# Performance work log

Measured on AMD Instinct MI355X. Metric: run time of the kernel, lower is better.

Reference implementation:

```python
import jax, jax.numpy as jnp
import numpy as np
import math
from jax import lax

NUM_POS = 128        # random_choice in pos_neg_sampling
NUM_TOT = 256        # pos + (128 + negative_padding) always totals 256
POS_W = 10.0         # positive_weight in compute_loss


def _conv(x, w, b, pad):
    y = lax.conv_general_dilated(x, w, (1, 1), pad,
                                 dimension_numbers=('NCHW', 'OIHW', 'NCHW'))
    return y + b[None, :, None, None]


def make_anchor_box(img_h, img_w, gh, gw):
    # torch.range(0, W, W/(gw-1)) == inclusive linspace with gw points
    xs = jnp.linspace(0.0, float(img_w), gw)
    ys = jnp.linspace(0.0, float(img_h), gh)
    gx, gy = jnp.meshgrid(xs, ys, indexing='ij')          # (gw, gh) like torch.meshgrid
    xy = jnp.stack([gx.reshape(-1), gy.reshape(-1)], -1).reshape(gh, gw, 2)
    whs = []
    for area in (128 * 128, 256 * 256, 512 * 512):
        for wr, hr in ((1, 1), (2, 1), (1, 2)):
            u = math.sqrt(area / (wr * hr))
            whs.append((wr * u, hr * u))
    wh = jnp.asarray(whs, jnp.float32)                    # (9, 2)
    xy9 = jnp.broadcast_to(xy[:, :, None, :], (gh, gw, 9, 2))
    wh9 = jnp.broadcast_to(wh[None, None], (gh, gw, 9, 2))
    boxes = jnp.concatenate([xy9, xy9 + wh9], -1)         # x1,y1,x2,y2
    return boxes.reshape(-1, 4)


def pairwise_iou(t, a):
    # t: [T,4], a: [A,4], xyxy -> [T,A]
    lt = jnp.maximum(t[:, None, :2], a[None, :, :2])
    rb = jnp.minimum(t[:, None, 2:], a[None, :, 2:])
    wh = jnp.clip(rb - lt, 0.0)
    inter = wh[..., 0] * wh[..., 1]
    at = (t[:, 2] - t[:, 0]) * (t[:, 3] - t[:, 1])
    aa = (a[:, 2] - a[:, 0]) * (a[:, 3] - a[:, 1])
    return inter / (at[:, None] + aa[None, :] - inter)


def box_encode(anchor, bbox):
    awh = anchor[:, 2:] - anchor[:, :2]
    bwh = bbox[:, 2:] - bbox[:, :2]
    ac = anchor[:, :2] + awh / 2
    bc = bbox[:, :2] + bwh / 2
    dxy = (bc - ac) / awh
    dwh = jnp.log(bwh / awh)
    return jnp.concatenate([dxy, dwh], 1)


def rpn_forward(x, target, conv_w, conv_b, bbox_w, bbox_b, score_w, score_b,
                img_h, img_w):
    gh, gw = x.shape[-2], x.shape[-1]
    h = jax.nn.relu(_conv(x[None], conv_w, conv_b, 'SAME'))
    bbox = jax.nn.relu(_conv(h, bbox_w, bbox_b, 'VALID')).reshape(-1, 4)   # [A,4]
    score = jax.nn.relu(_conv(h, score_w, score_b, 'VALID')).reshape(-1, 2)  # [A,2]
    anchors = make_anchor_box(img_h, img_w, gh, gw)                        # [A,4]

    iou = pairwise_iou(target, anchors)                                    # [T,A]
    max_iou = iou.max(0)
    tgt_idx = jnp.argmax(iou, 0)

    # deterministic replacement for np.random.choice sampling (fixed shapes)
    pos_score = jnp.where(max_iou > 0.7, max_iou, -1.0)
    pos_vals, pos_idx = lax.top_k(pos_score, NUM_POS)
    pos_valid = pos_vals > 0.0
    n_pos = jnp.sum(pos_valid.astype(jnp.int32))

    neg_score = jnp.where(max_iou < 0.3, 1.0 - max_iou, -1.0)
    neg_vals, neg_idx = lax.top_k(neg_score, NUM_TOT)
    neg_valid = (neg_vals > 0.0) & (jnp.arange(NUM_TOT) < (NUM_TOT - n_pos))

    bbox_pred = bbox[pos_idx]                                              # [128,4]
    scores_sel = score[jnp.concatenate([pos_idx, neg_idx])]                # [384,2]
    valid = jnp.concatenate([pos_valid, neg_valid]).astype(jnp.float32)

    tgt_scores = jnp.concatenate([
        jnp.tile(jnp.asarray([[1.0, 0.0]], jnp.float32), (NUM_POS, 1)),
        jnp.tile(jnp.asarray([[0.0, 1.0]], jnp.float32), (NUM_TOT, 1))], 0)

    matched = target[tgt_idx[pos_idx]]
    treg = box_encode(anchors[pos_idx], matched)

    ce = -jnp.sum(tgt_scores * jax.nn.log_softmax(scores_sel, -1), -1)
    score_loss = jnp.sum(ce * valid) / jnp.maximum(jnp.sum(valid), 1.0)

    d = bbox_pred - treg
    sl1 = jnp.where(jnp.abs(d) < 1.0, 0.5 * d * d, jnp.abs(d) - 0.5)
    pm = pos_valid.astype(jnp.float32)[:, None]
    reg_loss = jnp.sum(sl1 * pm) / jnp.maximum(jnp.sum(pm) * 4.0, 1.0)

    return score_loss + POS_W * reg_loss


def setup_inputs():
    key = jax.random.key(0)
    ks = jax.random.split(key, 8)
    cin, gh, gw, nt = 512, 128, 128, 64
    x = jax.random.normal(ks[0], (cin, gh, gw), jnp.float32)
    cxy = jax.random.uniform(ks[1], (nt, 2), minval=300.0, maxval=1748.0)
    wh = jax.random.uniform(ks[2], (nt, 2), minval=64.0, maxval=512.0)
    target = jnp.concatenate([cxy - wh / 2, cxy + wh / 2], -1)
    conv_w = jax.random.normal(ks[3], (cin, cin, 3, 3), jnp.float32) * 0.02
    conv_b = jnp.zeros((cin,), jnp.float32)
    bbox_w = jax.random.normal(ks[4], (36, cin, 1, 1), jnp.float32) * 0.02
    bbox_b = jnp.zeros((36,), jnp.float32)
    score_w = jax.random.normal(ks[5], (18, cin, 1, 1), jnp.float32) * 0.02
    score_b = jnp.zeros((18,), jnp.float32)
    return {'x': x, 'target': target, 'conv_w': conv_w, 'conv_b': conv_b,
            'bbox_w': bbox_w, 'bbox_b': bbox_b, 'score_w': score_w,
            'score_b': score_b, 'img_h': 2048, 'img_w': 2048}


def reference(x, target, conv_w, conv_b, bbox_w, bbox_b, score_w, score_b,
              img_h, img_w):
    return rpn_forward(x, target, conv_w, conv_b, bbox_w, bbox_b,
                       score_w, score_b, img_h, img_w)
```

## Files before the change

### kernel.cpp

```cpp
#include <hip/hip_runtime.h>
#include <cstdint>
#include <cstddef>

typedef unsigned long long ull;
typedef __bf16 bf16x8 __attribute__((ext_vector_type(8)));
typedef float f32x4 __attribute__((ext_vector_type(4)));

#define NA     147456
#define NT     64
#define KDIM   4608
#define NTASK  1280
#define CAND_CAP 4096
#define KSPLIT 4
#define NIOUB  576
#define NTRB   2048
#define NPREP2 512
#define NZERO  197

#define OFF_WB2   0
#define OFF_XT    4718592
#define OFF_ZERO  22024192
#define OFF_H4    22302720
#define OFF_MIOU  32788480
#define OFF_CAND  33378304
#define OFF_CPB   34557952
#define OFF_CBZ   34560256
#define OFF_NPOS  34562560
#define OFF_TREG  34562576
#define OFF_TASKS 34564624
#define OFF_OUT   34569744

#define UANC 90.509667991878f
__device__ __constant__ float WKa[9] = {128.0f, 2.0f*UANC, UANC, 256.0f, 4.0f*UANC, 2.0f*UANC, 512.0f, 8.0f*UANC, 4.0f*UANC};
__device__ __constant__ float HKa[9] = {128.0f, UANC, 2.0f*UANC, 256.0f, 2.0f*UANC, 4.0f*UANC, 512.0f, 4.0f*UANC, 8.0f*UANC};

__device__ __forceinline__ float iou_one(float x1, float y1, float x2, float y2, float4 t) {
#pragma clang fp contract(off)
  float ltx = fmaxf(t.x, x1), lty = fmaxf(t.y, y1);
  float rbx = fminf(t.z, x2), rby = fminf(t.w, y2);
  float wx = fmaxf(rbx - ltx, 0.0f);
  float wy = fmaxf(rby - lty, 0.0f);
  float inter = wx * wy;
  float at = (t.z - t.x) * (t.w - t.y);
  float aa = (x2 - x1) * (y2 - y1);
  return inter / ((at + aa) - inter);
}

__device__ __forceinline__ unsigned short f2bf(float f) {
  unsigned int u = __float_as_uint(f);
  unsigned int r = (u + 0x7fffu + ((u >> 16) & 1u)) >> 16;
  return (unsigned short)r;
}

__device__ __forceinline__ int boff(int kcb) {
  int rk = kcb >> 6;
  int dy = (rk * 11) >> 5;
  int dxo = rk - dy * 3;
  return (dy * 130 + dxo) * 512 + (kcb & 63) * 8;
}

__global__ __launch_bounds__(256) void k_pi(const float* __restrict__ cw,
    unsigned short* __restrict__ Wb2, const float* __restrict__ x,
    unsigned short* __restrict__ xtb, unsigned short* __restrict__ zrg,
    const float* __restrict__ tgt, const int* __restrict__ imw,
    const int* __restrict__ imh, float* __restrict__ miou,
    ull* __restrict__ cand, int* __restrict__ cpb, int* __restrict__ cbz) {
  __shared__ __align__(16) char smem[20480];
  int blk = blockIdx.x;
  int tid = threadIdx.x;
  if (blk >= NIOUB + NTRB + NPREP2) {
    int g = (blk - (NIOUB + NTRB + NPREP2)) * 256 + tid;
    uint4 z = {0u, 0u, 0u, 0u};
    if (g < 17408) {
      *(uint4*)(zrg + g * 8) = z;
    } else {
      int h = g - 17408;
      int pixi = h >> 6, j = h & 63;
      int yy, xx;
      if (pixi < 260) { yy = (pixi < 130) ? 0 : 129; xx = (pixi < 130) ? pixi : pixi - 130; }
      else { int p2 = pixi - 260; if (p2 < 128) { yy = 1 + p2; xx = 0; } else { yy = p2 - 127; xx = 129; } }
      *(uint4*)(xtb + (size_t)(yy * 130 + xx) * 512 + j * 8) = z;
    }
    return;
  }
  if (blk >= NIOUB + NTRB) {
    float* row = (float*)smem;
    int m = blk - (NIOUB + NTRB);
    const float* src = cw + (size_t)m * KDIM;
    for (int f = tid; f < KDIM; f += 256) {
      int cin = f / 9;
      row[cin * 10 + (f - cin * 9)] = src[f];
    }
    __syncthreads();
    for (int kc = tid; kc < 576; kc += 256) {
      int r = kc >> 6, c8 = kc & 63;
      int base = c8 * 80 + r;
      unsigned short o[8];
      #pragma unroll
      for (int j = 0; j < 8; ++j) o[j] = f2bf(row[base + j * 10]);
      *(uint4*)(Wb2 + ((size_t)kc * 512 + m) * 8) = *(const uint4*)o;
    }
    return;
  }
  if (blk >= NIOUB) {
    float* tile = (float*)smem;
    int tb = blk - NIOUB;
    int pix0 = (tb & 255) * 64;
    int cin0 = (tb >> 8) * 64;
    int pr = tid & 15, cr = tid >> 4;
    #pragma unroll
    for (int i = 0; i < 4; ++i) {
      int cin = cr + i * 16;
      float4 v = *(const float4*)(x + (size_t)(cin0 + cin) * 16384 + pix0 + pr * 4);
      tile[cin * 65 + pr * 4 + 0] = v.x;
      tile[cin * 65 + pr * 4 + 1] = v.y;
      tile[cin * 65 + pr * 4 + 2] = v.z;
      tile[cin * 65 + pr * 4 + 3] = v.w;
    }
    __syncthreads();
    #pragma unroll
    for (int i = 0; i < 4; ++i) {
      int pix = cr + i * 16;
      int plin = pix0 + pix;
      int py = plin >> 7, px = plin & 127;
      unsigned short o[4] = {f2bf(tile[(pr * 4 + 0) * 65 + pix]),
                             f2bf(tile[(pr * 4 + 1) * 65 + pix]),
                             f2bf(tile[(pr * 4 + 2) * 65 + pix]),
                             f2bf(tile[(pr * 4 + 3) * 65 + pix])};
      *(uint2*)(xtb + (size_t)((py + 1) * 130 + (px + 1)) * 512 + cin0 + pr * 4) = *(const uint2*)o;
    }
    return;
  }
  float4* ts = (float4*)smem;
  int* wz = (int*)(smem + 1024);
  int* wc = wz + 4;
  if (tid < NT) ts[tid] = ((const float4*)tgt)[tid];
  __syncthreads();
  int a = blk * 256 + tid;
  int k = a % 9;
  int pq = a / 9;
  int p = pq >> 7, q = pq & 127;
  float dx = (float)(*imw) / 127.0f;
  float dyl = (float)(*imh) / 127.0f;
  float x1 = (float)p * dx, y1 = (float)q * dyl;
  float x2 = x1 + WKa[k], y2 = y1 + HKa[k];
  float best = -1.0f;
  #pragma unroll 8
  for (int t = 0; t < NT; ++t) best = fmaxf(best, iou_one(x1, y1, x2, y2, ts[t]));
  miou[a] = best;
  int lane = tid & 63, w = tid >> 6;
  ull bz = __ballot(best == 0.0f);
  bool isc = best > 0.7f;
  ull bc = __ballot(isc);
  if (lane == 0) { wz[w] = (int)__popcll(bz); wc[w] = (int)__popcll(bc); }
  __syncthreads();
  if (tid == 0) {
    cbz[blk] = wz[0] + wz[1] + wz[2] + wz[3];
    cpb[blk] = wc[0] + wc[1] + wc[2] + wc[3];
  }
  if (isc) {
    int woff = 0;
    for (int i = 0; i < w; ++i) woff += wc[i];
    int rank = woff + (int)__popcll(bc & ((1ull << lane) - 1ull));
    cand[blk * 256 + rank] = ((ull)__float_as_uint(best) << 32) | (ull)(0xFFFFFFFFu - (unsigned)a);
  }
}

__global__ __launch_bounds__(256) void k_sel(const ull* __restrict__ cand,
    const int* __restrict__ cpb, const float* __restrict__ miou,
    const int* __restrict__ cbz, const float* __restrict__ tgt,
    const int* __restrict__ imw, const int* __restrict__ imh,
    int* __restrict__ nposp, float* __restrict__ treg, int* __restrict__ tasks) {
  __shared__ ull keys[CAND_CAP];
  __shared__ ull bnd[1024];
  __shared__ int hist[1024];
  __shared__ int cpbL[576];
  __shared__ int base576[577];
  __shared__ int wtot[4];
  __shared__ int selCnt, bndCnt, Tbin, mAbove;
  __shared__ int posi[128];
  __shared__ int npS;
  __shared__ int nzbase[145];
  __shared__ float4 ts[NT];
  __shared__ int negA[256];
  __shared__ int wsum[4];
  int tid = threadIdx.x;
  int lane = tid & 63;
  if (tid < NT) ts[tid] = ((const float4*)tgt)[tid];
  for (int i = tid; i < 576; i += 256) cpbL[i] = cpb[i];
  for (int i = tid; i < 1024; i += 256) hist[i] = 0;
  __syncthreads();
  int e0 = 0, e1 = 0, sA = 0, scanA = 0;
  if (tid < 192) {
    e0 = cpbL[3 * tid]; e1 = cpbL[3 * tid + 1]; int e2 = cpbL[3 * tid + 2];
    sA = e0 + e1 + e2;
    scanA = sA;
    for (int off = 1; off < 64; off <<= 1) {
      int v = __shfl_up(scanA, off);
      if (lane >= off) scanA += v;
    }
    if (lane == 63) wtot[tid >> 6] = scanA;
  }
  __syncthreads();
  if (tid < 192) {
    int w = tid >> 6;
    int woff = 0;
    for (int i = 0; i < w; ++i) woff += wtot[i];
    int excl = woff + scanA - sA;
    base576[3 * tid]     = excl;
    base576[3 * tid + 1] = excl + e0;
    base576[3 * tid + 2] = excl + e0 + e1;
    if (tid == 191) base576[576] = excl + sA;
  }
  __syncthreads();
  int cnt = base576[576]; if (cnt > CAND_CAP) cnt = CAND_CAP;
  for (int i = tid; i < CAND_CAP; i += 256) if (i >= cnt) keys[i] = 0ull;
  for (int rk = tid; rk < cnt; rk += 256) {
    int lo = 0, hi = 576;
    while (hi - lo > 1) { int mid = (lo + hi) >> 1; if (base576[mid] <= rk) lo = mid; else hi = mid; }
    keys[rk] = cand[lo * 256 + (rk - base576[lo])];
  }
  __syncthreads();
  if (cnt <= 128) {
    if (tid < cnt) posi[tid] = (int)(0xFFFFFFFFu - (unsigned)(keys[tid] & 0xFFFFFFFFull));
    if (tid == 0) { npS = cnt; *nposp = cnt; }
  } else {
    for (int i = tid; i < cnt; i += 256) {
      unsigned ib = (unsigned)(keys[i] >> 32);
      atomicAdd(&hist[(ib - 0x3F333334u) >> 13], 1);
    }
    __syncthreads();
    if (tid < 64) {
      int s = 0;
      #pragma unroll
      for (int t = 0; t < 16; ++t) s += hist[tid * 16 + t];
      int S = s;
      #pragma unroll
      for (int off = 1; off < 64; off <<= 1) {
        int u = __shfl_down(S, off);
        if (tid + off < 64) S += u;
      }
      ull mask = __ballot(S >= 128);
      int g = 63 - __clzll(mask);
      int aboveS = __shfl(S, (g + 1 < 64) ? g + 1 : 63);
      if (g == 63) aboveS = 0;
      if (tid == 0) {
        int run = aboveS, T = g * 16 + 15;
        for (int b = g * 16 + 15; b >= g * 16; --b) {
          int h = hist[b];
          if (run + h >= 128) { T = b; break; }
          run += h;
        }
        Tbin = T; mAbove = run; selCnt = 0; bndCnt = 0;
      }
    }
    __syncthreads();
    int T = Tbin, m = mAbove;
    for (int i = tid; i < cnt; i += 256) {
      ull kk = keys[i];
      unsigned ib = (unsigned)(kk >> 32);
      int b = (int)((ib - 0x3F333334u) >> 13);
      if (b > T) {
        int r = atomicAdd(&selCnt, 1);
        posi[r] = (int)(0xFFFFFFFFu - (unsigned)(kk & 0xFFFFFFFFull));
      } else if (b == T) {
        int r = atomicAdd(&bndCnt, 1);
        if (r < 1024) bnd[r] = kk;
      }
    }
    __syncthreads();
    int B = bndCnt;
    int need = 128 - m;
    if (B <= 1024) {
      int n2 = 2; while (n2 < B) n2 <<= 1;
      for (int i = tid; i < n2; i += 256) if (i >= B) bnd[i] = 0ull;
      for (int size = 2; size <= n2; size <<= 1)
        for (int stride = size >> 1; stride > 0; stride >>= 1) {
          __syncthreads();
          for (int t = tid; t < n2 / 2; t += 256) {
            int i = 2 * t - (t & (stride - 1));
            int j = i + stride;
            ull a = bnd[i], b2 = bnd[j];
            bool desc = ((i & size) == 0);
            if (desc ? (a < b2) : (a > b2)) { bnd[i] = b2; bnd[j] = a; }
          }
        }
      __syncthreads();
      if (tid < need) posi[m + tid] = (int)(0xFFFFFFFFu - (unsigned)(bnd[tid] & 0xFFFFFFFFull));
    } else {
      for (int size = 2; size <= CAND_CAP; size <<= 1)
        for (int stride = size >> 1; stride > 0; stride >>= 1) {
          __syncthreads();
          for (int t = tid; t < CAND_CAP / 2; t += 256) {
            int i = 2 * t - (t & (stride - 1));
            int j = i + stride;
            ull a = keys[i], b2 = keys[j];
            bool desc = ((i & size) == 0);
            if (desc ? (a < b2) : (a > b2)) { keys[i] = b2; keys[j] = a; }
          }
        }
      __syncthreads();
      if (tid < 128) posi[tid] = (int)(0xFFFFFFFFu - (unsigned)(keys[tid] & 0xFFFFFFFFull));
    }
    if (tid == 0) { npS = 128; *nposp = 128; }
  }
  __syncthreads();
  int np = npS;
  int sB = 0, scanB = 0;
  if (tid < 144) {
    int4 cz4 = *(const int4*)(cbz + 4 * tid);
    sB = cz4.x + cz4.y + cz4.z + cz4.w;
    scanB = sB;
    for (int off = 1; off < 64; off <<= 1) {
      int v = __shfl_up(scanB, off);
      if (lane >= off) scanB += v;
    }
    bool last = (tid < 128) ? (lane == 63) : (tid == 143);
    if (last) wsum[tid >> 6] = scanB;
  }
  __syncthreads();
  if (tid < 144) {
    int w = tid >> 6;
    int woff = 0;
    for (int i = 0; i < w; ++i) woff += wsum[i];
    nzbase[tid] = woff + scanB - sB;
    if (tid == 143) nzbase[144] = woff + scanB;
  }
  __syncthreads();
  int w = tid >> 6;
  for (int j = 0; j < 144; ++j) {
    if (nzbase[j] >= 256) break;
    int a0 = j * 1024 + tid * 4;
    float4 m4 = *(const float4*)(miou + a0);
    int f0 = (m4.x == 0.0f), f1 = (m4.y == 0.0f), f2 = (m4.z == 0.0f), f3 = (m4.w == 0.0f);
    int tsum = f0 + f1 + f2 + f3;
    int scan = tsum;
    for (int off = 1; off < 64; off <<= 1) {
      int v = __shfl_up(scan, off);
      if (lane >= off) scan += v;
    }
    if (lane == 63) wsum[w] = scan;
    __syncthreads();
    int woff = nzbase[j];
    for (int i = 0; i < w; ++i) woff += wsum[i];
    int r = woff + scan - tsum;
    if (f0) { if (r < 256) negA[r] = a0;     r++; }
    if (f1) { if (r < 256) negA[r] = a0 + 1; r++; }
    if (f2) { if (r < 256) negA[r] = a0 + 2; r++; }
    if (f3) { if (r < 256) negA[r] = a0 + 3;      }
    __syncthreads();
  }
  __syncthreads();
  if (tid < np) {
    int a = posi[tid];
    int k = a % 9; int pq = a / 9; int p = pq >> 7, q = pq & 127;
    float dx = (float)(*imw) / 127.0f, dyl = (float)(*imh) / 127.0f;
    float x1 = (float)p * dx, y1 = (float)q * dyl;
    float x2 = x1 + WKa[k], y2 = y1 + HKa[k];
    float best = -1.0f; int bt = 0;
    for (int t = 0; t < NT; ++t) {
      float v = iou_one(x1, y1, x2, y2, ts[t]);
      if (v > best) { best = v; bt = t; }
    }
    float4 m = ts[bt];
    float aw = x2 - x1, ah = y2 - y1;
    float acx = x1 + aw * 0.5f, acy = y1 + ah * 0.5f;
    float bwd = m.z - m.x, bhd = m.w - m.y;
    float bcx = m.x + bwd * 0.5f, bcy = m.y + bhd * 0.5f;
    treg[tid * 4 + 0] = (bcx - acx) / aw;
    treg[tid * 4 + 1] = (bcy - acy) / ah;
    treg[tid * 4 + 2] = logf(bwd / aw);
    treg[tid * 4 + 3] = logf(bhd / ah);
  }
  for (int t = tid; t < NTASK; t += 256) {
    int rec = 0;
    if (t < 768) {
      int s = t / 6, jj = t - s * 6;
      if (s < np) {
        int a = posi[s];
        int f, wr, xx;
        if (jj < 4) { f = 4 * a; wr = f >> 14; xx = (f & 127) + jj; }
        else        { f = 2 * a; wr = 36 + (f >> 14); xx = (f & 127) + (jj - 4); }
        int yy = (f >> 7) & 127;
        rec = (int)(0x80000000u | ((unsigned)wr << 16) | ((unsigned)yy << 8) | (unsigned)xx);
      }
    } else {
      int s = (t - 768) >> 1, jj = (t - 768) & 1;
      if (s < 256 - np) {
        int a = negA[s];
        int f = 2 * a; int wr = 36 + (f >> 14); int yy = (f >> 7) & 127; int xx = (f & 127) + jj;
        rec = (int)(0x80000000u | ((unsigned)wr << 16) | ((unsigned)yy << 8) | (unsigned)xx);
      }
    }
    tasks[t] = rec;
  }
}

__global__ __launch_bounds__(256) void k_mfma(const unsigned short* __restrict__ Wb2,
    const unsigned short* __restrict__ xtb, const unsigned short* __restrict__ zrg,
    const int* __restrict__ tasks, const int* __restrict__ nposp,
    float* __restrict__ H4) {
  int npos = *nposp;
  int tt0 = blockIdx.x * 128;
  int posend = 6 * npos, negend = 768 + 2 * (256 - npos);
  if (!((tt0 < posend) || ((tt0 + 128 > 768) && (tt0 < negend)))) return;
  int c0 = blockIdx.y * 128;
  int ks = blockIdx.z;
  int tid = threadIdx.x;
  int wave = tid >> 6, lane = tid & 63;
  int quad = lane >> 4, r = lane & 15;
  int m_base = c0 + (wave & 1) * 64;
  int n_base = tt0 + (wave >> 1) * 64;
  int kc0 = ks * 144 + quad;
  const bf16x8* Ab = (const bf16x8*)Wb2 + ((size_t)kc0 * 512 + m_base + r);

  const unsigned short* Bp[4];
  #pragma unroll
  for (int ni = 0; ni < 4; ++ni) {
    int rec = tasks[n_base + ni * 16 + r];
    int pix = (rec < 0) ? (((rec >> 8) & 127) * 130 + (rec & 127)) : 0;
    const unsigned short* base = (rec < 0) ? xtb : zrg;
    Bp[ni] = base + (size_t)pix * 512 + quad * 8;
  }
  int kcb = ks * 144;

  f32x4 acc[4][4];
  #pragma unroll
  for (int i = 0; i < 4; ++i)
    #pragma unroll
    for (int j = 0; j < 4; ++j) acc[i][j] = (f32x4){0.f, 0.f, 0.f, 0.f};

  bf16x8 a[4], b[4];
  #pragma unroll
  for (int mi = 0; mi < 4; ++mi) a[mi] = Ab[mi * 16];
  int ob0 = boff(kcb);
  #pragma unroll
  for (int ni = 0; ni < 4; ++ni) b[ni] = *(const bf16x8*)(Bp[ni] + ob0);

  for (int s = 0; s < 36; ++s) {
    bf16x8 an[4], bn[4];
    if (s < 35) {
      const bf16x8* An = Ab + (size_t)(s + 1) * 4 * 512;
      int ob = boff(kcb + 4 * (s + 1));
      #pragma unroll
      for (int mi = 0; mi < 4; ++mi) an[mi] = An[mi * 16];
      #pragma unroll
      for (int ni = 0; ni < 4; ++ni) bn[ni] = *(const bf16x8*)(Bp[ni] + ob);
    }
    #pragma unroll
    for (int mi = 0; mi < 4; ++mi)
      #pragma unroll
      for (int ni = 0; ni < 4; ++ni)
        acc[mi][ni] = __builtin_amdgcn_mfma_f32_16x16x32_bf16(a[mi], b[ni], acc[mi][ni], 0, 0, 0);
    if (s < 35) {
      #pragma unroll
      for (int mi = 0; mi < 4; ++mi) a[mi] = an[mi];
      #pragma unroll
      for (int ni = 0; ni < 4; ++ni) b[ni] = bn[ni];
    }
  }
  size_t hb = (size_t)ks * NTASK;
  #pragma unroll
  for (int mi = 0; mi < 4; ++mi) {
    int c = m_base + mi * 16 + quad * 4;
    #pragma unroll
    for (int ni = 0; ni < 4; ++ni) {
      int t = n_base + ni * 16 + r;
      *(f32x4*)(H4 + (hb + t) * 512 + c) = acc[mi][ni];
    }
  }
}

__global__ __launch_bounds__(256) void k_out(const float* __restrict__ H4,
    const int* __restrict__ tasks,
    const float* __restrict__ cb, const float* __restrict__ bw,
    const float* __restrict__ bb, const float* __restrict__ sw,
    const float* __restrict__ sb, float* __restrict__ outv) {
  int wave = threadIdx.x >> 6, lane = threadIdx.x & 63;
  int t = blockIdx.x * 4 + wave;
  int rec = tasks[t];
  if (rec >= 0) return;
  int wr = (rec >> 16) & 63;
  const float* wrow = (wr < 36) ? (bw + wr * 512) : (sw + (wr - 36) * 512);
  float s = 0.0f;
  #pragma unroll
  for (int it = 0; it < 8; ++it) {
    int c = it * 64 + lane;
    size_t o = (size_t)t * 512 + c;
    float hv = H4[o] + H4[o + 1280 * 512] + H4[o + 2 * 1280 * 512] + H4[o + 3 * 1280 * 512] + cb[c];
    s = fmaf(fmaxf(hv, 0.0f), wrow[c], s);
  }
  #pragma unroll
  for (int off = 32; off > 0; off >>= 1) s += __shfl_down(s, off);
  if (lane == 0) {
    float b = (wr < 36) ? bb[wr] : sb[wr - 36];
    outv[t] = fmaxf(s + b, 0.0f);
  }
}

__global__ __launch_bounds__(256) void k_loss(const float* __restrict__ outv,
    const float* __restrict__ treg, const int* __restrict__ nposp,
    float* __restrict__ out) {
  __shared__ float r1[256], r2[256];
  int tid = threadIdx.x;
  int np = *nposp;
  float ce = 0.0f;
  for (int r = tid; r < 384; r += 256) {
    bool valid = (r < 128) ? (r < np) : ((r - 128) < 256 - np);
    if (valid) {
      int t0 = (r < 128) ? (r * 6 + 4) : (768 + 2 * (r - 128));
      float s0 = outv[t0], s1 = outv[t0 + 1];
      float mm = fmaxf(s0, s1);
      float lse = mm + logf(expf(s0 - mm) + expf(s1 - mm));
      ce += lse - ((r < 128) ? s0 : s1);
    }
  }
  float rg = 0.0f;
  for (int r = tid; r < 512; r += 256) {
    if ((r >> 2) < np) {
      float d = outv[(r >> 2) * 6 + (r & 3)] - treg[r];
      float ad = fabsf(d);
      rg += (ad < 1.0f) ? 0.5f * d * d : ad - 0.5f;
    }
  }
  r1[tid] = ce; r2[tid] = rg;
  __syncthreads();
  for (int s = 128; s > 0; s >>= 1) {
    if (tid < s) { r1[tid] += r1[tid + s]; r2[tid] += r2[tid + s]; }
    __syncthreads();
  }
  if (tid == 0) {
    float score_loss = r1[0] / 256.0f;
    float reg_loss = r2[0] / fmaxf(4.0f * (float)np, 1.0f);
    out[0] = score_loss + 10.0f * reg_loss;
  }
}

extern "C" void kernel_launch(void* const* d_in, const int* in_sizes, int n_in,
                              void* d_out, int out_size, void* d_ws, size_t ws_size,
                              hipStream_t stream) {
  const float* x   = (const float*)d_in[0];
  const float* tgt = (const float*)d_in[1];
  const float* cw  = (const float*)d_in[2];
  const float* cb  = (const float*)d_in[3];
  const float* bw  = (const float*)d_in[4];
  const float* bb  = (const float*)d_in[5];
  const float* sw  = (const float*)d_in[6];
  const float* sb  = (const float*)d_in[7];
  const int* imh   = (const int*)d_in[8];
  const int* imw   = (const int*)d_in[9];

  char* ws = (char*)d_ws;
  unsigned short* Wb2 = (unsigned short*)(ws + OFF_WB2);
  unsigned short* xtb = (unsigned short*)(ws + OFF_XT);
  unsigned short* zrg = (unsigned short*)(ws + OFF_ZERO);
  float* H4    = (float*)(ws + OFF_H4);
  float* miou  = (float*)(ws + OFF_MIOU);
  ull*   cand  = (ull*)(ws + OFF_CAND);
  int*   cpb   = (int*)(ws + OFF_CPB);
  int*   cbz   = (int*)(ws + OFF_CBZ);
  int*   nposp = (int*)(ws + OFF_NPOS);
  float* treg  = (float*)(ws + OFF_TREG);
  int*   tasks = (int*)(ws + OFF_TASKS);
  float* outv  = (float*)(ws + OFF_OUT);
  float* out   = (float*)d_out;

  k_pi   <<<dim3(NIOUB + NTRB + NPREP2 + NZERO), dim3(256), 0, stream>>>(cw, Wb2, x, xtb, zrg, tgt, imw, imh, miou, cand, cpb, cbz);
  k_sel  <<<dim3(1),              dim3(256), 0, stream>>>(cand, cpb, miou, cbz, tgt, imw, imh, nposp, treg, tasks);
  k_mfma <<<dim3(10, 4, KSPLIT),  dim3(256), 0, stream>>>(Wb2, xtb, zrg, tasks, nposp, H4);
  k_out  <<<dim3(320),            dim3(256), 0, stream>>>(H4, tasks, cb, bw, bb, sw, sb, outv);
  k_loss <<<dim3(1),              dim3(256), 0, stream>>>(outv, treg, nposp, out);
}
```

Baseline: 156.0 us.

## Fuse selection into MFMA kernel via spin flag and fold loss into output kernel

Merges the single-block selection kernel into the MFMA GEMM launch: one designated block runs selection and publishes tasks through a global flag, while the other blocks prefetch their weight slices into cache and spin-wait on it. The loss reduction is folded into the output kernel using per-block atomicAdd to the output, which is zeroed in the first kernel. The K-split drops from 4 to 2 with twice the steps per block, cutting partial-sum traffic. This removes two kernel launches and their serialization, but relies on all GEMM blocks being co-resident, reuses the zero-region as a flag, and makes the float loss sum order nondeterministic.

```diff
diff --git a/kernel.cpp b/kernel.cpp
--- a/kernel.cpp
+++ b/kernel.cpp
@@ -11,7 +11,8 @@
 #define KDIM   4608
 #define NTASK  1280
 #define CAND_CAP 4096
-#define KSPLIT 4
+#define KSPLIT 2
+#define NSTEP  72
 #define NIOUB  576
 #define NTRB   2048
 #define NPREP2 512
@@ -28,7 +29,6 @@
 #define OFF_NPOS  34562560
 #define OFF_TREG  34562576
 #define OFF_TASKS 34564624
-#define OFF_OUT   34569744
 
 #define UANC 90.509667991878f
 __device__ __constant__ float WKa[9] = {128.0f, 2.0f*UANC, UANC, 256.0f, 4.0f*UANC, 2.0f*UANC, 512.0f, 8.0f*UANC, 4.0f*UANC};
@@ -64,13 +64,15 @@
     unsigned short* __restrict__ xtb, unsigned short* __restrict__ zrg,
     const float* __restrict__ tgt, const int* __restrict__ imw,
     const int* __restrict__ imh, float* __restrict__ miou,
-    ull* __restrict__ cand, int* __restrict__ cpb, int* __restrict__ cbz) {
+    ull* __restrict__ cand, int* __restrict__ cpb, int* __restrict__ cbz,
+    float* __restrict__ out0) {
   __shared__ __align__(16) char smem[20480];
   int blk = blockIdx.x;
   int tid = threadIdx.x;
   if (blk >= NIOUB + NTRB + NPREP2) {
     int g = (blk - (NIOUB + NTRB + NPREP2)) * 256 + tid;
     uint4 z = {0u, 0u, 0u, 0u};
+    if (g == 0) *out0 = 0.0f;
     if (g < 17408) {
       *(uint4*)(zrg + g * 8) = z;
     } else {
@@ -166,11 +168,14 @@
   }
 }
 
-__global__ __launch_bounds__(256) void k_sel(const ull* __restrict__ cand,
-    const int* __restrict__ cpb, const float* __restrict__ miou,
-    const int* __restrict__ cbz, const float* __restrict__ tgt,
-    const int* __restrict__ imw, const int* __restrict__ imh,
-    int* __restrict__ nposp, float* __restrict__ treg, int* __restrict__ tasks) {
+__global__ __launch_bounds__(256) void k_mfma(const unsigned short* __restrict__ Wb2,
+    const unsigned short* __restrict__ xtb, unsigned short* __restrict__ zrg,
+    const ull* __restrict__ cand, const int* __restrict__ cpb,
+    const float* __restrict__ miou, const int* __restrict__ cbz,
+    const float* __restrict__ tgt, const int* __restrict__ imw,
+    const int* __restrict__ imh,
+    int* __restrict__ nposp, float* __restrict__ treg, int* __restrict__ tasks,
+    float* __restrict__ H4) {
   __shared__ ull keys[CAND_CAP];
   __shared__ ull bnd[1024];
   __shared__ int hist[1024];
@@ -184,234 +189,251 @@
   __shared__ float4 ts[NT];
   __shared__ int negA[256];
   __shared__ int wsum[4];
+
   int tid = threadIdx.x;
-  int lane = tid & 63;
-  if (tid < NT) ts[tid] = ((const float4*)tgt)[tid];
-  for (int i = tid; i < 576; i += 256) cpbL[i] = cpb[i];
-  for (int i = tid; i < 1024; i += 256) hist[i] = 0;
-  __syncthreads();
-  int e0 = 0, e1 = 0, sA = 0, scanA = 0;
-  if (tid < 192) {
-    e0 = cpbL[3 * tid]; e1 = cpbL[3 * tid + 1]; int e2 = cpbL[3 * tid + 2];
-    sA = e0 + e1 + e2;
-    scanA = sA;
-    for (int off = 1; off < 64; off <<= 1) {
-      int v = __shfl_up(scanA, off);
-      if (lane >= off) scanA += v;
-    }
-    if (lane == 63) wtot[tid >> 6] = scanA;
-  }
-  __syncthreads();
-  if (tid < 192) {
+  int* flag = (int*)zrg;
+  bool isSel = (blockIdx.x == 9 && blockIdx.y == 3 && blockIdx.z == 1);
+
+  if (isSel) {
+    int lane = tid & 63;
+    if (tid < NT) ts[tid] = ((const float4*)tgt)[tid];
+    for (int i = tid; i < 576; i += 256) cpbL[i] = cpb[i];
+    for (int i = tid; i < 1024; i += 256) hist[i] = 0;
+    __syncthreads();
+    int e0 = 0, e1 = 0, sA = 0, scanA = 0;
+    if (tid < 192) {
+      e0 = cpbL[3 * tid]; e1 = cpbL[3 * tid + 1]; int e2 = cpbL[3 * tid + 2];
+      sA = e0 + e1 + e2;
+      scanA = sA;
+      for (int off = 1; off < 64; off <<= 1) {
+        int v = __shfl_up(scanA, off);
+        if (lane >= off) scanA += v;
+      }
+      if (lane == 63) wtot[tid >> 6] = scanA;
+    }
+    __syncthreads();
+    if (tid < 192) {
+      int w = tid >> 6;
+      int woff = 0;
+      for (int i = 0; i < w; ++i) woff += wtot[i];
+      int excl = woff + scanA - sA;
+      base576[3 * tid]     = excl;
+      base576[3 * tid + 1] = excl + e0;
+      base576[3 * tid + 2] = excl + e0 + e1;
+      if (tid == 191) base576[576] = excl + sA;
+    }
+    __syncthreads();
+    int cnt = base576[576]; if (cnt > CAND_CAP) cnt = CAND_CAP;
+    for (int i = tid; i < CAND_CAP; i += 256) if (i >= cnt) keys[i] = 0ull;
+    for (int rk = tid; rk < cnt; rk += 256) {
+      int lo = 0, hi = 576;
+      while (hi - lo > 1) { int mid = (lo + hi) >> 1; if (base576[mid] <= rk) lo = mid; else hi = mid; }
+      keys[rk] = cand[lo * 256 + (rk - base576[lo])];
+    }
+    __syncthreads();
+    if (cnt <= 128) {
+      if (tid < cnt) posi[tid] = (int)(0xFFFFFFFFu - (unsigned)(keys[tid] & 0xFFFFFFFFull));
+      if (tid == 0) { npS = cnt; *nposp = cnt; }
+    } else {
+      for (int i = tid; i < cnt; i += 256) {
+        unsigned ib = (unsigned)(keys[i] >> 32);
+        atomicAdd(&hist[(ib - 0x3F333334u) >> 13], 1);
+      }
+      __syncthreads();
+      if (tid < 64) {
+        int s = 0;
+        #pragma unroll
+        for (int t = 0; t < 16; ++t) s += hist[tid * 16 + t];
+        int S = s;
+        #pragma unroll
+        for (int off = 1; off < 64; off <<= 1) {
+          int u = __shfl_down(S, off);
+          if (tid + off < 64) S += u;
+        }
+        ull mask = __ballot(S >= 128);
+        int g = 63 - __clzll(mask);
+        int aboveS = __shfl(S, (g + 1 < 64) ? g + 1 : 63);
+        if (g == 63) aboveS = 0;
+        if (tid == 0) {
+          int run = aboveS, T = g * 16 + 15;
+          for (int b = g * 16 + 15; b >= g * 16; --b) {
+            int h = hist[b];
+            if (run + h >= 128) { T = b; break; }
+            run += h;
+          }
+          Tbin = T; mAbove = run; selCnt = 0; bndCnt = 0;
+        }
+      }
+      __syncthreads();
+      int T = Tbin, m = mAbove;
+      for (int i = tid; i < cnt; i += 256) {
+        ull kk = keys[i];
+        unsigned ib = (unsigned)(kk >> 32);
+        int b = (int)((ib - 0x3F333334u) >> 13);
+        if (b > T) {
+          int r = atomicAdd(&selCnt, 1);
+          posi[r] = (int)(0xFFFFFFFFu - (unsigned)(kk & 0xFFFFFFFFull));
+        } else if (b == T) {
+          int r = atomicAdd(&bndCnt, 1);
+          if (r < 1024) bnd[r] = kk;
+        }
+      }
+      __syncthreads();
+      int B = bndCnt;
+      int need = 128 - m;
+      if (B <= 1024) {
+        int n2 = 2; while (n2 < B) n2 <<= 1;
+        for (int i = tid; i < n2; i += 256) if (i >= B) bnd[i] = 0ull;
+        for (int size = 2; size <= n2; size <<= 1)
+          for (int stride = size >> 1; stride > 0; stride >>= 1) {
+            __syncthreads();
+            for (int t = tid; t < n2 / 2; t += 256) {
+              int i = 2 * t - (t & (stride - 1));
+              int j = i + stride;
+              ull a = bnd[i], b2 = bnd[j];
+              bool desc = ((i & size) == 0);
+              if (desc ? (a < b2) : (a > b2)) { bnd[i] = b2; bnd[j] = a; }
+            }
+          }
+        __syncthreads();
+        if (tid < need) posi[m + tid] = (int)(0xFFFFFFFFu - (unsigned)(bnd[tid] & 0xFFFFFFFFull));
+      } else {
+        for (int size = 2; size <= CAND_CAP; size <<= 1)
+          for (int stride = size >> 1; stride > 0; stride >>= 1) {
+            __syncthreads();
+            for (int t = tid; t < CAND_CAP / 2; t += 256) {
+              int i = 2 * t - (t & (stride - 1));
+              int j = i + stride;
+              ull a = keys[i], b2 = keys[j];
+              bool desc = ((i & size) == 0);
+              if (desc ? (a < b2) : (a > b2)) { keys[i] = b2; keys[j] = a; }
+            }
+          }
+        __syncthreads();
+        if (tid < 128) posi[tid] = (int)(0xFFFFFFFFu - (unsigned)(keys[tid] & 0xFFFFFFFFull));
+      }
+      if (tid == 0) { npS = 128; *nposp = 128; }
+    }
+    __syncthreads();
+    int np = npS;
+    int sB = 0, scanB = 0;
+    if (tid < 144) {
+      int4 cz4 = *(const int4*)(cbz + 4 * tid);
+      sB = cz4.x + cz4.y + cz4.z + cz4.w;
+      scanB = sB;
+      for (int off = 1; off < 64; off <<= 1) {
+        int v = __shfl_up(scanB, off);
+        if (lane >= off) scanB += v;
+      }
+      bool last = (tid < 128) ? (lane == 63) : (tid == 143);
+      if (last) wsum[tid >> 6] = scanB;
+    }
+    __syncthreads();
+    if (tid < 144) {
+      int w = tid >> 6;
+      int woff = 0;
+      for (int i = 0; i < w; ++i) woff += wsum[i];
+      nzbase[tid] = woff + scanB - sB;
+      if (tid == 143) nzbase[144] = woff + scanB;
+    }
+    __syncthreads();
     int w = tid >> 6;
-    int woff = 0;
-    for (int i = 0; i < w; ++i) woff += wtot[i];
-    int excl = woff + scanA - sA;
-    base576[3 * tid]     = excl;
-    base576[3 * tid + 1] = excl + e0;
-    base576[3 * tid + 2] = excl + e0 + e1;
-    if (tid == 191) base576[576] = excl + sA;
-  }
-  __syncthreads();
-  int cnt = base576[576]; if (cnt > CAND_CAP) cnt = CAND_CAP;
-  for (int i = tid; i < CAND_CAP; i += 256) if (i >= cnt) keys[i] = 0ull;
-  for (int rk = tid; rk < cnt; rk += 256) {
-    int lo = 0, hi = 576;
-    while (hi - lo > 1) { int mid = (lo + hi) >> 1; if (base576[mid] <= rk) lo = mid; else hi = mid; }
-    keys[rk] = cand[lo * 256 + (rk - base576[lo])];
-  }
-  __syncthreads();
-  if (cnt <= 128) {
-    if (tid < cnt) posi[tid] = (int)(0xFFFFFFFFu - (unsigned)(keys[tid] & 0xFFFFFFFFull));
-    if (tid == 0) { npS = cnt; *nposp = cnt; }
+    for (int j = 0; j < 144; ++j) {
+      if (nzbase[j] >= 256) break;
+      int a0 = j * 1024 + tid * 4;
+      float4 m4 = *(const float4*)(miou + a0);
+      int f0 = (m4.x == 0.0f), f1 = (m4.y == 0.0f), f2 = (m4.z == 0.0f), f3 = (m4.w == 0.0f);
+      int tsum = f0 + f1 + f2 + f3;
+      int scan = tsum;
+      for (int off = 1; off < 64; off <<= 1) {
+        int v = __shfl_up(scan, off);
+        if (lane >= off) scan += v;
+      }
+      if (lane == 63) wsum[w] = scan;
+      __syncthreads();
+      int woff = nzbase[j];
+      for (int i = 0; i < w; ++i) woff += wsum[i];
+      int r = woff + scan - tsum;
+      if (f0) { if (r < 256) negA[r] = a0;     r++; }
+      if (f1) { if (r < 256) negA[r] = a0 + 1; r++; }
+      if (f2) { if (r < 256) negA[r] = a0 + 2; r++; }
+      if (f3) { if (r < 256) negA[r] = a0 + 3;      }
+      __syncthreads();
+    }
+    __syncthreads();
+    if (tid < np) {
+      int a = posi[tid];
+      int k = a % 9; int pq = a / 9; int p = pq >> 7, q = pq & 127;
+      float dx = (float)(*imw) / 127.0f, dyl = (float)(*imh) / 127.0f;
+      float x1 = (float)p * dx, y1 = (float)q * dyl;
+      float x2 = x1 + WKa[k], y2 = y1 + HKa[k];
+      float best = -1.0f; int bt = 0;
+      for (int t = 0; t < NT; ++t) {
+        float v = iou_one(x1, y1, x2, y2, ts[t]);
+        if (v > best) { best = v; bt = t; }
+      }
+      float4 m = ts[bt];
+      float aw = x2 - x1, ah = y2 - y1;
+      float acx = x1 + aw * 0.5f, acy = y1 + ah * 0.5f;
+      float bwd = m.z - m.x, bhd = m.w - m.y;
+      float bcx = m.x + bwd * 0.5f, bcy = m.y + bhd * 0.5f;
+      treg[tid * 4 + 0] = (bcx - acx) / aw;
+      treg[tid * 4 + 1] = (bcy - acy) / ah;
+      treg[tid * 4 + 2] = logf(bwd / aw);
+      treg[tid * 4 + 3] = logf(bhd / ah);
+    }
+    for (int t = tid; t < NTASK; t += 256) {
+      int rec = 0;
+      if (t < 768) {
+        int s = t / 6, jj = t - s * 6;
+        if (s < np) {
+          int a = posi[s];
+          int f, wr, xx;
+          if (jj < 4) { f = 4 * a; wr = f >> 14; xx = (f & 127) + jj; }
+          else        { f = 2 * a; wr = 36 + (f >> 14); xx = (f & 127) + (jj - 4); }
+          int yy = (f >> 7) & 127;
+          rec = (int)(0x80000000u | ((unsigned)wr << 16) | ((unsigned)yy << 8) | (unsigned)xx);
+        }
+      } else {
+        int s = (t - 768) >> 1, jj = (t - 768) & 1;
+        if (s < 256 - np) {
+          int a = negA[s];
+          int f = 2 * a; int wr = 36 + (f >> 14); int yy = (f >> 7) & 127; int xx = (f & 127) + jj;
+          rec = (int)(0x80000000u | ((unsigned)wr << 16) | ((unsigned)yy << 8) | (unsigned)xx);
+        }
+      }
+      tasks[t] = rec;
+    }
+    __threadfence();
+    __syncthreads();
+    if (tid == 0) atomicExch(flag, 1);
   } else {
-    for (int i = tid; i < cnt; i += 256) {
-      unsigned ib = (unsigned)(keys[i] >> 32);
-      atomicAdd(&hist[(ib - 0x3F333334u) >> 13], 1);
-    }
-    __syncthreads();
-    if (tid < 64) {
-      int s = 0;
-      #pragma unroll
-      for (int t = 0; t < 16; ++t) s += hist[tid * 16 + t];
-      int S = s;
-      #pragma unroll
-      for (int off = 1; off < 64; off <<= 1) {
-        int u = __shfl_down(S, off);
-        if (tid + off < 64) S += u;
-      }
-      ull mask = __ballot(S >= 128);
-      int g = 63 - __clzll(mask);
-      int aboveS = __shfl(S, (g + 1 < 64) ? g + 1 : 63);
-      if (g == 63) aboveS = 0;
-      if (tid == 0) {
-        int run = aboveS, T = g * 16 + 15;
-        for (int b = g * 16 + 15; b >= g * 16; --b) {
-          int h = hist[b];
-          if (run + h >= 128) { T = b; break; }
-          run += h;
-        }
-        Tbin = T; mAbove = run; selCnt = 0; bndCnt = 0;
-      }
-    }
-    __syncthreads();
-    int T = Tbin, m = mAbove;
-    for (int i = tid; i < cnt; i += 256) {
-      ull kk = keys[i];
-      unsigned ib = (unsigned)(kk >> 32);
-      int b = (int)((ib - 0x3F333334u) >> 13);
-      if (b > T) {
-        int r = atomicAdd(&selCnt, 1);
-        posi[r] = (int)(0xFFFFFFFFu - (unsigned)(kk & 0xFFFFFFFFull));
-      } else if (b == T) {
-        int r = atomicAdd(&bndCnt, 1);
-        if (r < 1024) bnd[r] = kk;
-      }
-    }
-    __syncthreads();
-    int B = bndCnt;
-    int need = 128 - m;
-    if (B <= 1024) {
-      int n2 = 2; while (n2 < B) n2 <<= 1;
-      for (int i = tid; i < n2; i += 256) if (i >= B) bnd[i] = 0ull;
-      for (int size = 2; size <= n2; size <<= 1)
-        for (int stride = size >> 1; stride > 0; stride >>= 1) {
-          __syncthreads();
-          for (int t = tid; t < n2 / 2; t += 256) {
-            int i = 2 * t - (t & (stride - 1));
-            int j = i + stride;
-            ull a = bnd[i], b2 = bnd[j];
-            bool desc = ((i & size) == 0);
-            if (desc ? (a < b2) : (a > b2)) { bnd[i] = b2; bnd[j] = a; }
-          }
-        }
-      __syncthreads();
-      if (tid < need) posi[m + tid] = (int)(0xFFFFFFFFu - (unsigned)(bnd[tid] & 0xFFFFFFFFull));
-    } else {
-      for (int size = 2; size <= CAND_CAP; size <<= 1)
-        for (int stride = size >> 1; stride > 0; stride >>= 1) {
-          __syncthreads();
-          for (int t = tid; t < CAND_CAP / 2; t += 256) {
-            int i = 2 * t - (t & (stride - 1));
-            int j = i + stride;
-            ull a = keys[i], b2 = keys[j];
-            bool desc = ((i & size) == 0);
-            if (desc ? (a < b2) : (a > b2)) { keys[i] = b2; keys[j] = a; }
-          }
-        }
-      __syncthreads();
-      if (tid < 128) posi[tid] = (int)(0xFFFFFFFFu - (unsigned)(keys[tid] & 0xFFFFFFFFull));
-    }
-    if (tid == 0) { npS = 128; *nposp = 128; }
-  }
-  __syncthreads();
-  int np = npS;
-  int sB = 0, scanB = 0;
-  if (tid < 144) {
-    int4 cz4 = *(const int4*)(cbz + 4 * tid);
-    sB = cz4.x + cz4.y + cz4.z + cz4.w;
-    scanB = sB;
-    for (int off = 1; off < 64; off <<= 1) {
-      int v = __shfl_up(scanB, off);
-      if (lane >= off) scanB += v;
-    }
-    bool last = (tid < 128) ? (lane == 63) : (tid == 143);
-    if (last) wsum[tid >> 6] = scanB;
-  }
-  __syncthreads();
-  if (tid < 144) {
-    int w = tid >> 6;
-    int woff = 0;
-    for (int i = 0; i < w; ++i) woff += wsum[i];
-    nzbase[tid] = woff + scanB - sB;
-    if (tid == 143) nzbase[144] = woff + scanB;
-  }
-  __syncthreads();
-  int w = tid >> 6;
-  for (int j = 0; j < 144; ++j) {
-    if (nzbase[j] >= 256) break;
-    int a0 = j * 1024 + tid * 4;
-    float4 m4 = *(const float4*)(miou + a0);
-    int f0 = (m4.x == 0.0f), f1 = (m4.y == 0.0f), f2 = (m4.z == 0.0f), f3 = (m4.w == 0.0f);
-    int tsum = f0 + f1 + f2 + f3;
-    int scan = tsum;
-    for (int off = 1; off < 64; off <<= 1) {
-      int v = __shfl_up(scan, off);
-      if (lane >= off) scan += v;
-    }
-    if (lane == 63) wsum[w] = scan;
-    __syncthreads();
-    int woff = nzbase[j];
-    for (int i = 0; i < w; ++i) woff += wsum[i];
-    int r = woff + scan - tsum;
-    if (f0) { if (r < 256) negA[r] = a0;     r++; }
-    if (f1) { if (r < 256) negA[r] = a0 + 1; r++; }
-    if (f2) { if (r < 256) negA[r] = a0 + 2; r++; }
-    if (f3) { if (r < 256) negA[r] = a0 + 3;      }
-    __syncthreads();
-  }
-  __syncthreads();
-  if (tid < np) {
-    int a = posi[tid];
-    int k = a % 9; int pq = a / 9; int p = pq >> 7, q = pq & 127;
-    float dx = (float)(*imw) / 127.0f, dyl = (float)(*imh) / 127.0f;
-    float x1 = (float)p * dx, y1 = (float)q * dyl;
-    float x2 = x1 + WKa[k], y2 = y1 + HKa[k];
-    float best = -1.0f; int bt = 0;
-    for (int t = 0; t < NT; ++t) {
-      float v = iou_one(x1, y1, x2, y2, ts[t]);
-      if (v > best) { best = v; bt = t; }
-    }
-    float4 m = ts[bt];
-    float aw = x2 - x1, ah = y2 - y1;
-    float acx = x1 + aw * 0.5f, acy = y1 + ah * 0.5f;
-    float bwd = m.z - m.x, bhd = m.w - m.y;
-    float bcx = m.x + bwd * 0.5f, bcy = m.y + bhd * 0.5f;
-    treg[tid * 4 + 0] = (bcx - acx) / aw;
-    treg[tid * 4 + 1] = (bcy - acy) / ah;
-    treg[tid * 4 + 2] = logf(bwd / aw);
-    treg[tid * 4 + 3] = logf(bhd / ah);
-  }
-  for (int t = tid; t < NTASK; t += 256) {
-    int rec = 0;
-    if (t < 768) {
-      int s = t / 6, jj = t - s * 6;
-      if (s < np) {
-        int a = posi[s];
-        int f, wr, xx;
-        if (jj < 4) { f = 4 * a; wr = f >> 14; xx = (f & 127) + jj; }
-        else        { f = 2 * a; wr = 36 + (f >> 14); xx = (f & 127) + (jj - 4); }
-        int yy = (f >> 7) & 127;
-        rec = (int)(0x80000000u | ((unsigned)wr << 16) | ((unsigned)yy << 8) | (unsigned)xx);
-      }
-    } else {
-      int s = (t - 768) >> 1, jj = (t - 768) & 1;
-      if (s < 256 - np) {
-        int a = negA[s];
-        int f = 2 * a; int wr = 36 + (f >> 14); int yy = (f >> 7) & 127; int xx = (f & 127) + jj;
-        rec = (int)(0x80000000u | ((unsigned)wr << 16) | ((unsigned)yy << 8) | (unsigned)xx);
-      }
-    }
-    tasks[t] = rec;
-  }
-}
-
-__global__ __launch_bounds__(256) void k_mfma(const unsigned short* __restrict__ Wb2,
-    const unsigned short* __restrict__ xtb, const unsigned short* __restrict__ zrg,
-    const int* __restrict__ tasks, const int* __restrict__ nposp,
-    float* __restrict__ H4) {
+    int c0p = blockIdx.y * 128;
+    int kbase = blockIdx.z * 288;
+    unsigned accp = 0;
+    for (int i = tid; i < 288 * 32; i += 256) {
+      int kc = i >> 5, mq = (i & 31) * 4;
+      accp ^= *(const unsigned*)(Wb2 + ((size_t)(kbase + kc) * 512 + c0p + mq) * 8);
+    }
+    asm volatile("" :: "v"(accp));
+    if (tid == 0) {
+      while (atomicCAS(flag, 2, 2) == 0) __builtin_amdgcn_s_sleep(32);
+    }
+    __syncthreads();
+    __threadfence();
+  }
+
   int npos = *nposp;
   int tt0 = blockIdx.x * 128;
   int posend = 6 * npos, negend = 768 + 2 * (256 - npos);
   if (!((tt0 < posend) || ((tt0 + 128 > 768) && (tt0 < negend)))) return;
   int c0 = blockIdx.y * 128;
   int ks = blockIdx.z;
-  int tid = threadIdx.x;
   int wave = tid >> 6, lane = tid & 63;
   int quad = lane >> 4, r = lane & 15;
   int m_base = c0 + (wave & 1) * 64;
   int n_base = tt0 + (wave >> 1) * 64;
-  int kc0 = ks * 144 + quad;
+  int kc0 = ks * 288 + quad;
   const bf16x8* Ab = (const bf16x8*)Wb2 + ((size_t)kc0 * 512 + m_base + r);
 
   const unsigned short* Bp[4];
@@ -422,7 +444,7 @@
     const unsigned short* base = (rec < 0) ? xtb : zrg;
     Bp[ni] = base + (size_t)pix * 512 + quad * 8;
   }
-  int kcb = ks * 144;
+  int kcb = ks * 288;
 
   f32x4 acc[4][4];
   #pragma unroll
@@ -437,9 +459,9 @@
   #pragma unroll
   for (int ni = 0; ni < 4; ++ni) b[ni] = *(const bf16x8*)(Bp[ni] + ob0);
 
-  for (int s = 0; s < 36; ++s) {
+  for (int s = 0; s < NSTEP; ++s) {
     bf16x8 an[4], bn[4];
-    if (s < 35) {
+    if (s < NSTEP - 1) {
       const bf16x8* An = Ab + (size_t)(s + 1) * 4 * 512;
       int ob = boff(kcb + 4 * (s + 1));
       #pragma unroll
@@ -452,7 +474,7 @@
       #pragma unroll
       for (int ni = 0; ni < 4; ++ni)
         acc[mi][ni] = __builtin_amdgcn_mfma_f32_16x16x32_bf16(a[mi], b[ni], acc[mi][ni], 0, 0, 0);
-    if (s < 35) {
+    if (s < NSTEP - 1) {
       #pragma unroll
       for (int mi = 0; mi < 4; ++mi) a[mi] = an[mi];
       #pragma unroll
@@ -475,64 +497,64 @@
     const int* __restrict__ tasks,
     const float* __restrict__ cb, const float* __restrict__ bw,
     const float* __restrict__ bb, const float* __restrict__ sw,
-    const float* __restrict__ sb, float* __restrict__ outv) {
+    const float* __restrict__ sb, const float* __restrict__ treg,
+    const int* __restrict__ nposp, float* __restrict__ out) {
+  __shared__ float sOut[4];
+  __shared__ float sContrib[4];
   int wave = threadIdx.x >> 6, lane = threadIdx.x & 63;
   int t = blockIdx.x * 4 + wave;
   int rec = tasks[t];
-  if (rec >= 0) return;
-  int wr = (rec >> 16) & 63;
-  const float* wrow = (wr < 36) ? (bw + wr * 512) : (sw + (wr - 36) * 512);
-  float s = 0.0f;
-  #pragma unroll
-  for (int it = 0; it < 8; ++it) {
-    int c = it * 64 + lane;
-    size_t o = (size_t)t * 512 + c;
-    float hv = H4[o] + H4[o + 1280 * 512] + H4[o + 2 * 1280 * 512] + H4[o + 3 * 1280 * 512] + cb[c];
-    s = fmaf(fmaxf(hv, 0.0f), wrow[c], s);
-  }
-  #pragma unroll
-  for (int off = 32; off > 0; off >>= 1) s += __shfl_down(s, off);
+  float outval = 0.0f;
+  if (rec < 0) {
+    int wr = (rec >> 16) & 63;
+    const float* wrow = (wr < 36) ? (bw + wr * 512) : (sw + (wr - 36) * 512);
+    float s = 0.0f;
+    #pragma unroll
+    for (int it = 0; it < 8; ++it) {
+      int c = it * 64 + lane;
+      size_t o = (size_t)t * 512 + c;
+      float hv = H4[o] + H4[o + 1280 * 512] + cb[c];
+      s = fmaf(fmaxf(hv, 0.0f), wrow[c], s);
+    }
+    #pragma unroll
+    for (int off = 32; off > 0; off >>= 1) s += __shfl_down(s, off);
+    if (lane == 0) {
+      float b = (wr < 36) ? bb[wr] : sb[wr - 36];
+      outval = fmaxf(s + b, 0.0f);
+    }
+  }
+  if (lane == 0) sOut[wave] = outval;
+  __syncthreads();
   if (lane == 0) {
-    float b = (wr < 36) ? bb[wr] : sb[wr - 36];
-    outv[t] = fmaxf(s + b, 0.0f);
-  }
-}
-
-__global__ __launch_bounds__(256) void k_loss(const float* __restrict__ outv,
-    const float* __restrict__ treg, const int* __restrict__ nposp,
-    float* __restrict__ out) {
-  __shared__ float r1[256], r2[256];
-  int tid = threadIdx.x;
-  int np = *nposp;
-  float ce = 0.0f;
-  for (int r = tid; r < 384; r += 256) {
-    bool valid = (r < 128) ? (r < np) : ((r - 128) < 256 - np);
-    if (valid) {
-      int t0 = (r < 128) ? (r * 6 + 4) : (768 + 2 * (r - 128));
-      float s0 = outv[t0], s1 = outv[t0 + 1];
-      float mm = fmaxf(s0, s1);
-      float lse = mm + logf(expf(s0 - mm) + expf(s1 - mm));
-      ce += lse - ((r < 128) ? s0 : s1);
-    }
-  }
-  float rg = 0.0f;
-  for (int r = tid; r < 512; r += 256) {
-    if ((r >> 2) < np) {
-      float d = outv[(r >> 2) * 6 + (r & 3)] - treg[r];
-      float ad = fabsf(d);
-      rg += (ad < 1.0f) ? 0.5f * d * d : ad - 0.5f;
-    }
-  }
-  r1[tid] = ce; r2[tid] = rg;
+    float contrib = 0.0f;
+    if (rec < 0) {
+      if (t < 768) {
+        int s6 = t / 6, j = t - s6 * 6;
+        if (j < 4) {
+          int np = *nposp;
+          float d = outval - treg[s6 * 4 + j];
+          float ad = fabsf(d);
+          float sl1 = (ad < 1.0f) ? 0.5f * d * d : ad - 0.5f;
+          contrib = 10.0f * sl1 / fmaxf(4.0f * (float)np, 1.0f);
+        } else if (j == 4) {
+          float s0 = outval, s1 = sOut[wave + 1];
+          float mm = fmaxf(s0, s1);
+          float lse = mm + logf(expf(s0 - mm) + expf(s1 - mm));
+          contrib = (lse - s0) * (1.0f / 256.0f);
+        }
+      } else if (((t - 768) & 1) == 0) {
+        float s0 = outval, s1 = sOut[wave + 1];
+        float mm = fmaxf(s0, s1);
+        float lse = mm + logf(expf(s0 - mm) + expf(s1 - mm));
+        contrib = (lse - s1) * (1.0f / 256.0f);
+      }
+    }
+    sContrib[wave] = contrib;
+  }
   __syncthreads();
-  for (int s = 128; s > 0; s >>= 1) {
-    if (tid < s) { r1[tid] += r1[tid + s]; r2[tid] += r2[tid + s]; }
-    __syncthreads();
-  }
-  if (tid == 0) {
-    float score_loss = r1[0] / 256.0f;
-    float reg_loss = r2[0] / fmaxf(4.0f * (float)np, 1.0f);
-    out[0] = score_loss + 10.0f * reg_loss;
+  if (threadIdx.x == 0) {
+    float c = sContrib[0] + sContrib[1] + sContrib[2] + sContrib[3];
+    if (c != 0.0f) atomicAdd(out, c);
   }
 }
 
@@ -562,12 +584,9 @@
   int*   nposp = (int*)(ws + OFF_NPOS);
   float* treg  = (float*)(ws + OFF_TREG);
   int*   tasks = (int*)(ws + OFF_TASKS);
-  float* outv  = (float*)(ws + OFF_OUT);
   float* out   = (float*)d_out;
 
-  k_pi   <<<dim3(NIOUB + NTRB + NPREP2 + NZERO), dim3(256), 0, stream>>>(cw, Wb2, x, xtb, zrg, tgt, imw, imh, miou, cand, cpb, cbz);
-  k_sel  <<<dim3(1),              dim3(256), 0, stream>>>(cand, cpb, miou, cbz, tgt, imw, imh, nposp, treg, tasks);
-  k_mfma <<<dim3(10, 4, KSPLIT),  dim3(256), 0, stream>>>(Wb2, xtb, zrg, tasks, nposp, H4);
-  k_out  <<<dim3(320),            dim3(256), 0, stream>>>(H4, tasks, cb, bw, bb, sw, sb, outv);
-  k_loss <<<dim3(1),              dim3(256), 0, stream>>>(outv, treg, nposp, out);
-}
+  k_pi   <<<dim3(NIOUB + NTRB + NPREP2 + NZERO), dim3(256), 0, stream>>>(cw, Wb2, x, xtb, zrg, tgt, imw, imh, miou, cand, cpb, cbz, out);
+  k_mfma <<<dim3(10, 4, KSPLIT),  dim3(256), 0, stream>>>(Wb2, xtb, zrg, cand, cpb, miou, cbz, tgt, imw, imh, nposp, treg, tasks, H4);
+  k_out  <<<dim3(320),            dim3(256), 0, stream>>>(H4, tasks, cb, bw, bb, sw, sb, treg, nposp, out);
+}
```

Result: slower. 179.9 us (+15.3%).
